# Optimization experiments

Measured on AMD Instinct MI355X. Metric: run time of the kernel, lower is better.

## Reference

```python
import jax, jax.numpy as jnp
import numpy as np

H = 1024
B = 8
T = 2048

def setup_inputs() -> dict:
    key = jax.random.key(0)
    ks = jax.random.split(key, 12)
    s = 1.0 / np.sqrt(H)
    return {
        "x": jax.random.normal(ks[0], (B, T, H), dtype=jnp.float32),
        "time_decay": jax.random.normal(ks[1], (H,), dtype=jnp.float32) * 0.1,
        "time_first": jax.random.normal(ks[2], (H,), dtype=jnp.float32) * 0.1,
        "time_mix_key": jax.random.uniform(ks[3], (1, 1, H), dtype=jnp.float32),
        "time_mix_value": jax.random.uniform(ks[4], (1, 1, H), dtype=jnp.float32),
        "time_mix_receptance": jax.random.uniform(ks[5], (1, 1, H), dtype=jnp.float32),
        "Wk": jax.random.normal(ks[6], (H, H), dtype=jnp.float32) * s,
        "Wv": jax.random.normal(ks[7], (H, H), dtype=jnp.float32) * s,
        "Wr": jax.random.normal(ks[8], (H, H), dtype=jnp.float32) * s,
        "Wo": jax.random.normal(ks[9], (H, H), dtype=jnp.float32) * s,
        "bo": jax.random.normal(ks[10], (H,), dtype=jnp.float32) * 0.01,
    }

def reference(x, time_decay, time_first, time_mix_key, time_mix_value,
              time_mix_receptance, Wk, Wv, Wr, Wo, bo):
    # time shift: shifted[:, t] = x[:, t-1], shifted[:, 0] = 0
    shifted = jnp.pad(x, ((0, 0), (1, 0), (0, 0)))[:, :-1]
    k_in = x * time_mix_key + shifted * (1.0 - time_mix_key)
    v_in = x * time_mix_value + shifted * (1.0 - time_mix_value)
    r_in = x * time_mix_receptance + shifted * (1.0 - time_mix_receptance)
    k = jnp.einsum('bth,oh->bto', k_in, Wk)
    v = jnp.einsum('bth,oh->bto', v_in, Wv)
    r = jax.nn.sigmoid(jnp.einsum('bth,oh->bto', r_in, Wr))

    td = jnp.exp(-jnp.exp(time_decay))  # (H,)

    def step(carry, kv):
        num, den = carry            # (B, H) each
        k_t, v_t = kv               # (B, H) each
        e = jnp.exp(time_first + k_t)
        out_t = (num + e * v_t) / (den + e)
        ek = jnp.exp(k_t)
        return (td * num + ek * v_t, td * den + ek), out_t

    init = (jnp.zeros((x.shape[0], x.shape[2]), x.dtype),
            jnp.zeros((x.shape[0], x.shape[2]), x.dtype))
    # scan over time: (T, B, H)
    _, wkv = jax.lax.scan(step, init, (k.transpose(1, 0, 2), v.transpose(1, 0, 2)))
    wkv = wkv.transpose(1, 0, 2)    # (B, T, H)

    return jnp.einsum('bth,oh->bto', r * wkv, Wo) + bo
```

## Files before the change

kernel.cpp:

```cpp
#include <hip/hip_runtime.h>
#include <hip/hip_bf16.h>
#include <cstdint>
#include <cstddef>

#define HH 1024
#define BB 8
#define TT 2048
#define MM (BB*TT)
#define CC 128
#define LL (TT/CC)

typedef __attribute__((ext_vector_type(8))) short bf16x8;
typedef __attribute__((ext_vector_type(8))) unsigned short u16x8;
typedef __attribute__((ext_vector_type(4))) float f32x4;

__device__ __forceinline__ unsigned short f2bf(float f) {
  union { float f; unsigned u; } v; v.f = f;
  return (unsigned short)((v.u + 0x7fffu + ((v.u >> 16) & 1u)) >> 16);
}
__device__ __forceinline__ float bf2f(unsigned short s) {
  union { float f; unsigned u; } v; v.u = ((unsigned)s) << 16;
  return v.f;
}

__device__ __forceinline__ void load_lds16(const void* g, void* l) {
  __builtin_amdgcn_global_load_lds((const __attribute__((address_space(1))) void*)g,
                                   (__attribute__((address_space(3))) void*)l,
                                   16, 0, 0);
}

__global__ __launch_bounds__(256) void prep(const float* __restrict__ x,
    const float* __restrict__ tmk, const float* __restrict__ tmv, const float* __restrict__ tmr,
    const float* __restrict__ Wk, const float* __restrict__ Wv,
    const float* __restrict__ Wr, const float* __restrict__ Wo,
    unsigned short* __restrict__ kin, unsigned short* __restrict__ vin,
    unsigned short* __restrict__ rin, unsigned short* __restrict__ Wbf) {
  const int bx = blockIdx.x;
  if (bx < 16384) {
    const int gid = bx * 256 + threadIdx.x;
    const size_t e0 = (size_t)gid * 4;
    const int h = (int)(e0 & (HH - 1));
    const int t = (int)((e0 >> 10) & (TT - 1));
    const float4 xv = *(const float4*)(x + e0);
    float4 sv = make_float4(0.f, 0.f, 0.f, 0.f);
    if (t != 0) sv = *(const float4*)(x + e0 - HH);
    const float4 k4 = *(const float4*)(tmk + h);
    const float4 v4 = *(const float4*)(tmv + h);
    const float4 r4 = *(const float4*)(tmr + h);
    ushort4 ko, vo, ro;
    ko.x = f2bf(sv.x + k4.x * (xv.x - sv.x)); ko.y = f2bf(sv.y + k4.y * (xv.y - sv.y));
    ko.z = f2bf(sv.z + k4.z * (xv.z - sv.z)); ko.w = f2bf(sv.w + k4.w * (xv.w - sv.w));
    vo.x = f2bf(sv.x + v4.x * (xv.x - sv.x)); vo.y = f2bf(sv.y + v4.y * (xv.y - sv.y));
    vo.z = f2bf(sv.z + v4.z * (xv.z - sv.z)); vo.w = f2bf(sv.w + v4.w * (xv.w - sv.w));
    ro.x = f2bf(sv.x + r4.x * (xv.x - sv.x)); ro.y = f2bf(sv.y + r4.y * (xv.y - sv.y));
    ro.z = f2bf(sv.z + r4.z * (xv.z - sv.z)); ro.w = f2bf(sv.w + r4.w * (xv.w - sv.w));
    *(ushort4*)(kin + e0) = ko;
    *(ushort4*)(vin + e0) = vo;
    *(ushort4*)(rin + e0) = ro;
  } else {
    const int q = bx - 16384;
    const int zz = q >> 10;
    const float* src = zz == 0 ? Wk : zz == 1 ? Wv : zz == 2 ? Wr : Wo;
    const int i = ((q & 1023) * 256 + threadIdx.x) * 4;
    const float4 v = *(const float4*)(src + i);
    ushort4 o; o.x = f2bf(v.x); o.y = f2bf(v.y); o.z = f2bf(v.z); o.w = f2bf(v.w);
    *(ushort4*)(Wbf + (size_t)zz * HH * HH + i) = o;
  }
}


#define BAR()   do { asm volatile("" ::: "memory"); __builtin_amdgcn_s_barrier(); \
                     asm volatile("" ::: "memory"); } while (0)
#define VM6()   asm volatile("s_waitcnt vmcnt(6)" ::: "memory")
#define VM0()   asm volatile("s_waitcnt vmcnt(0)" ::: "memory")
#define PRIO1() __builtin_amdgcn_s_setprio(1)
#define PRIO0() __builtin_amdgcn_s_setprio(0)

__device__ __forceinline__ void stA(const unsigned short* __restrict__ Ag, int m0, int kt,
                                    unsigned short* buf, int h, int w, int rl, int scol) {
#pragma unroll
  for (int l = 0; l < 2; ++l) {
    const int row = l * 128 + h * 64 + w * 8;
    load_lds16(Ag + (size_t)(m0 + row + rl) * HH + kt + scol, buf + row * 64);
  }
}
__device__ __forceinline__ void stB(const unsigned short* __restrict__ Bg, int n0, int kt,
                                    unsigned short* buf, int h, int w, int rl, int scol) {
#pragma unroll
  for (int l = 0; l < 2; ++l) {
    const int row = (2 * (l * 2 + (w >> 2)) + h) * 32 + (w & 3) * 8;
    load_lds16(Bg + (size_t)(n0 + row + rl) * HH + kt + scol, buf + row * 64);
  }
}

template<int MH>
__device__ __forceinline__ void rdA(const unsigned short* buf, bf16x8 (&af)[4][2],
                                    int wm, int l15, int kq, int swz) {
#pragma unroll
  for (int kk = 0; kk < 2; ++kk)
#pragma unroll
    for (int fm = 0; fm < 4; ++fm)
      af[fm][kk] = *(const bf16x8*)(buf + (wm * 128 + MH * 64 + fm * 16 + l15) * 64
                                        + ((kk * 32 + kq * 8) ^ swz));
}
template<int NH>
__device__ __forceinline__ void rdB(const unsigned short* buf, bf16x8 (&bfr)[2][2][2],
                                    int wn, int l15, int kq, int swz) {
#pragma unroll
  for (int kk = 0; kk < 2; ++kk)
#pragma unroll
    for (int fn = 0; fn < 2; ++fn)
      bfr[NH][fn][kk] = *(const bf16x8*)(buf + (wn * 64 + NH * 32 + fn * 16 + l15) * 64
                                             + ((kk * 32 + kq * 8) ^ swz));
}
template<int MH, int NH>
__device__ __forceinline__ void mfmaQ(f32x4 (&acc)[8][4], const bf16x8 (&af)[4][2],
                                      const bf16x8 (&bfr)[2][2][2]) {
#pragma unroll
  for (int kk = 0; kk < 2; ++kk)
#pragma unroll
    for (int fm = 0; fm < 4; ++fm)
#pragma unroll
      for (int fn = 0; fn < 2; ++fn)
        acc[MH * 4 + fm][NH * 2 + fn] = __builtin_amdgcn_mfma_f32_16x16x32_bf16(
            bfr[NH][fn][kk], af[fm][kk], acc[MH * 4 + fm][NH * 2 + fn], 0, 0, 0);
}

__device__ __forceinline__ void gemm256(const unsigned short* __restrict__ Ag,
                                        const unsigned short* __restrict__ Bg,
                                        const int m0, const int n0,
                                        unsigned short* As, unsigned short* Bs,
                                        f32x4 (&acc)[8][4]) {
  const int tid = threadIdx.x;
  const int lane = tid & 63;
  const int w = tid >> 6;
  const int wm = w >> 2, wn = w & 3;
  const int l15 = lane & 15, kq = lane >> 4;
  const int swz = (l15 & 7) << 3;
  const int rl = lane >> 3;
  const int scol = ((lane & 7) ^ rl) * 8;
  unsigned short* const A0 = As;
  unsigned short* const A1 = As + 256 * 64;
  unsigned short* const B0 = Bs;
  unsigned short* const B1 = Bs + 256 * 64;
  bf16x8 af[4][2], bfr[2][2][2];

  stA(Ag, m0, 0, A0, 0, w, rl, scol);
  stB(Bg, n0, 0, B0, 0, w, rl, scol);
  stB(Bg, n0, 0, B0, 1, w, rl, scol);
  stA(Ag, m0, 0, A0, 1, w, rl, scol);
  stA(Ag, m0, 64, A1, 0, w, rl, scol);
  stB(Bg, n0, 64, B1, 0, w, rl, scol);
  stB(Bg, n0, 64, B1, 1, w, rl, scol);
  VM6(); BAR();

#pragma unroll 1
  for (int i = 0; i < 8; ++i) {
    const int tb1 = ((2 * i + 1) * 64) & (HH - 1);
    const int tn0 = ((2 * i + 2) * 64) & (HH - 1);
    const int tn1 = ((2 * i + 3) * 64) & (HH - 1);
    rdB<0>(B0, bfr, wn, l15, kq, swz);
    rdA<0>(A0, af, wm, l15, kq, swz);
    stA(Ag, m0, tb1, A1, 1, w, rl, scol);
    BAR(); PRIO1(); mfmaQ<0, 0>(acc, af, bfr); PRIO0(); BAR();
    rdB<1>(B0, bfr, wn, l15, kq, swz);
    stA(Ag, m0, tn0, A0, 0, w, rl, scol);
    BAR(); PRIO1(); mfmaQ<0, 1>(acc, af, bfr); PRIO0(); BAR();
    rdA<1>(A0, af, wm, l15, kq, swz);
    stB(Bg, n0, tn0, B0, 0, w, rl, scol);
    BAR(); PRIO1(); mfmaQ<1, 1>(acc, af, bfr); PRIO0(); BAR();
    stB(Bg, n0, tn0, B0, 1, w, rl, scol);
    VM6(); BAR(); PRIO1(); mfmaQ<1, 0>(acc, af, bfr); PRIO0(); BAR();
    rdB<0>(B1, bfr, wn, l15, kq, swz);
    rdA<0>(A1, af, wm, l15, kq, swz);
    stA(Ag, m0, tn0, A0, 1, w, rl, scol);
    BAR(); PRIO1(); mfmaQ<0, 0>(acc, af, bfr); PRIO0(); BAR();
    rdB<1>(B1, bfr, wn, l15, kq, swz);
    stA(Ag, m0, tn1, A1, 0, w, rl, scol);
    BAR(); PRIO1(); mfmaQ<0, 1>(acc, af, bfr); PRIO0(); BAR();
    rdA<1>(A1, af, wm, l15, kq, swz);
    stB(Bg, n0, tn1, B1, 0, w, rl, scol);
    BAR(); PRIO1(); mfmaQ<1, 1>(acc, af, bfr); PRIO0(); BAR();
    stB(Bg, n0, tn1, B1, 1, w, rl, scol);
    VM6(); BAR(); PRIO1(); mfmaQ<1, 0>(acc, af, bfr); PRIO0(); BAR();
  }
  VM0();
}

__device__ __forceinline__ void swizzle_mn256(int x, int& m0, int& n0) {
  const int wg = (x & 7) * 32 + (x >> 3);
  m0 = (wg >> 2) * 256;
  n0 = (wg & 3) * 256;
}

__global__ __launch_bounds__(512, 2) void gemm_kvr(const unsigned short* __restrict__ kin,
    const unsigned short* __restrict__ vin, const unsigned short* __restrict__ rin,
    const unsigned short* __restrict__ Wbf,
    unsigned short* __restrict__ kb, unsigned short* __restrict__ vb,
    unsigned short* __restrict__ rb) {
  __shared__ unsigned short As[2 * 256 * 64];
  __shared__ unsigned short Bs[2 * 256 * 64];
  const int z = blockIdx.y;
  const unsigned short* Ag = z == 0 ? kin : (z == 1 ? vin : rin);
  const unsigned short* Bg = Wbf + (size_t)z * HH * HH;
  unsigned short* Cg = z == 0 ? kb : (z == 1 ? vb : rb);
  int m0, n0; swizzle_mn256(blockIdx.x, m0, n0);
  f32x4 acc[8][4] = {};
  gemm256(Ag, Bg, m0, n0, As, Bs, acc);
  const int lane = threadIdx.x & 63, w = threadIdx.x >> 6;
  const int wm = w >> 2, wn = w & 3, l15 = lane & 15, lq = lane >> 4;
  const bool sig = (z == 2);
#pragma unroll
  for (int fm = 0; fm < 8; ++fm) {
    const size_t mrow = (size_t)(m0 + wm * 128 + fm * 16 + l15) * HH;
#pragma unroll
    for (int fn = 0; fn < 4; ++fn) {
      const int ncol = n0 + wn * 64 + fn * 16 + lq * 4;
      float v0 = acc[fm][fn][0], v1 = acc[fm][fn][1];
      float v2 = acc[fm][fn][2], v3 = acc[fm][fn][3];
      if (sig) {
        v0 = 1.0f / (1.0f + __expf(-v0)); v1 = 1.0f / (1.0f + __expf(-v1));
        v2 = 1.0f / (1.0f + __expf(-v2)); v3 = 1.0f / (1.0f + __expf(-v3));
      }
      ushort4 o; o.x = f2bf(v0); o.y = f2bf(v1); o.z = f2bf(v2); o.w = f2bf(v3);
      *(ushort4*)(Cg + mrow + ncol) = o;
    }
  }
}

__global__ __launch_bounds__(512, 2) void gemm_o(const unsigned short* __restrict__ Ag,
    const unsigned short* __restrict__ Bg, const float* __restrict__ bias,
    float* __restrict__ C) {
  __shared__ unsigned short As[2 * 256 * 64];
  __shared__ unsigned short Bs[2 * 256 * 64];
  int m0, n0; swizzle_mn256(blockIdx.x, m0, n0);
  f32x4 acc[8][4] = {};
  gemm256(Ag, Bg, m0, n0, As, Bs, acc);
  const int lane = threadIdx.x & 63, w = threadIdx.x >> 6;
  const int wm = w >> 2, wn = w & 3, l15 = lane & 15, lq = lane >> 4;
#pragma unroll
  for (int fm = 0; fm < 8; ++fm) {
    const size_t mrow = (size_t)(m0 + wm * 128 + fm * 16 + l15) * HH;
#pragma unroll
    for (int fn = 0; fn < 4; ++fn) {
      const int ncol = n0 + wn * 64 + fn * 16 + lq * 4;
      const float4 bv = *(const float4*)(bias + ncol);
      float4 ov;
      ov.x = acc[fm][fn][0] + bv.x; ov.y = acc[fm][fn][1] + bv.y;
      ov.z = acc[fm][fn][2] + bv.z; ov.w = acc[fm][fn][3] + bv.w;
      *(float4*)(C + mrow + ncol) = ov;
    }
  }
}

__global__ __launch_bounds__(256) void wkv_part(const unsigned short* __restrict__ k,
    const unsigned short* __restrict__ v, const float* __restrict__ tdec,
    float* __restrict__ pnum, float* __restrict__ pden) {
  const int gid = blockIdx.x * 256 + threadIdx.x;
  const int h0 = (gid & 127) * 8;
  const int b = (gid >> 7) & (BB - 1);
  const int c = gid >> 10;
  float td[8], num[8], den[8];
#pragma unroll
  for (int j = 0; j < 8; ++j) {
    td[j] = __expf(-__expf(tdec[h0 + j]));
    num[j] = 0.f; den[j] = 0.f;
  }
  size_t idx = (size_t)b * TT * HH + (size_t)(c * LL) * HH + h0;
#pragma unroll 4
  for (int i = 0; i < LL; ++i, idx += HH) {
    const u16x8 k8 = *(const u16x8*)(k + idx);
    const u16x8 v8 = *(const u16x8*)(v + idx);
#pragma unroll
    for (int j = 0; j < 8; ++j) {
      const float ek = __expf(bf2f(k8[j]));
      num[j] = td[j] * num[j] + ek * bf2f(v8[j]);
      den[j] = td[j] * den[j] + ek;
    }
  }
  const size_t o = (size_t)c * (BB * HH) + b * HH + h0;
#pragma unroll
  for (int j = 0; j < 8; ++j) { pnum[o + j] = num[j]; pden[o + j] = den[j]; }
}

__global__ __launch_bounds__(256) void wkv_scan(const float* __restrict__ tdec,
    float* __restrict__ pnum, float* __restrict__ pden) {
  const int bh = blockIdx.x * 256 + threadIdx.x;
  const int h = bh & (HH - 1);
  const float ed = __expf(tdec[h]);
  const float tdL = __expf(-ed * (float)LL);
  float num = 0.f, den = 0.f;
#pragma unroll 8
  for (int c = 0; c < CC; ++c) {
    const size_t o = (size_t)c * (BB * HH) + bh;
    const float tn = pnum[o], td_ = pden[o];
    pnum[o] = num; pden[o] = den;
    num = tdL * num + tn;
    den = tdL * den + td_;
  }
}

__global__ __launch_bounds__(256) void wkv_final(const unsigned short* __restrict__ k,
    const unsigned short* __restrict__ v, const unsigned short* __restrict__ r,
    const float* __restrict__ tdec, const float* __restrict__ tfst,
    const float* __restrict__ pnum, const float* __restrict__ pden,
    unsigned short* __restrict__ rwkv) {
  const int gid = blockIdx.x * 256 + threadIdx.x;
  const int h0 = (gid & 127) * 8;
  const int b = (gid >> 7) & (BB - 1);
  const int c = gid >> 10;
  float td[8], etf[8], num[8], den[8];
  const size_t o = (size_t)c * (BB * HH) + b * HH + h0;
#pragma unroll
  for (int j = 0; j < 8; ++j) {
    td[j] = __expf(-__expf(tdec[h0 + j]));
    etf[j] = __expf(tfst[h0 + j]);
    num[j] = pnum[o + j]; den[j] = pden[o + j];
  }
  size_t idx = (size_t)b * TT * HH + (size_t)(c * LL) * HH + h0;
#pragma unroll 2
  for (int i = 0; i < LL; ++i, idx += HH) {
    const u16x8 k8 = *(const u16x8*)(k + idx);
    const u16x8 v8 = *(const u16x8*)(v + idx);
    const u16x8 r8 = *(const u16x8*)(r + idx);
    u16x8 o8;
#pragma unroll
    for (int j = 0; j < 8; ++j) {
      const float ek = __expf(bf2f(k8[j]));
      const float vt = bf2f(v8[j]);
      const float rt = bf2f(r8[j]);
      const float e = ek * etf[j];
      const float inv = __builtin_amdgcn_rcpf(den[j] + e);
      const float outv = (num[j] + e * vt) * inv;
      num[j] = td[j] * num[j] + ek * vt;
      den[j] = td[j] * den[j] + ek;
      o8[j] = f2bf(outv * rt);
    }
    *(u16x8*)(rwkv + idx) = o8;
  }
}

extern "C" void kernel_launch(void* const* d_in, const int* in_sizes, int n_in,
                              void* d_out, int out_size, void* d_ws, size_t ws_size,
                              hipStream_t stream) {
  (void)in_sizes; (void)n_in; (void)out_size; (void)ws_size;
  const float* x    = (const float*)d_in[0];
  const float* tdec = (const float*)d_in[1];
  const float* tfst = (const float*)d_in[2];
  const float* tmk  = (const float*)d_in[3];
  const float* tmv  = (const float*)d_in[4];
  const float* tmr  = (const float*)d_in[5];
  const float* Wk   = (const float*)d_in[6];
  const float* Wv   = (const float*)d_in[7];
  const float* Wr   = (const float*)d_in[8];
  const float* Wo   = (const float*)d_in[9];
  const float* bo   = (const float*)d_in[10];
  float* out = (float*)d_out;

  char* ws = (char*)d_ws;
  const size_t MiB = (size_t)1 << 20;
  unsigned short* Wbf = (unsigned short*)(ws);
  unsigned short* kin = (unsigned short*)(ws + 8 * MiB);
  unsigned short* vin = (unsigned short*)(ws + 40 * MiB);
  unsigned short* rin = (unsigned short*)(ws + 72 * MiB);
  unsigned short* rb  = (unsigned short*)(ws + 104 * MiB);
  unsigned short* kb = (unsigned short*)out;
  unsigned short* vb = kb + (size_t)MM * HH;
  unsigned short* rwkv = kin;
  float* pnum = (float*)(ws + 40 * MiB);
  float* pden = (float*)(ws + 44 * MiB);

  hipLaunchKernelGGL(prep, dim3(20480), dim3(256), 0, stream,
                     x, tmk, tmv, tmr, Wk, Wv, Wr, Wo, kin, vin, rin, Wbf);
  hipLaunchKernelGGL(gemm_kvr, dim3(256, 3), dim3(512), 0, stream,
                     kin, vin, rin, Wbf, kb, vb, rb);
  hipLaunchKernelGGL(wkv_part, dim3(512), dim3(256), 0, stream,
                     kb, vb, tdec, pnum, pden);
  hipLaunchKernelGGL(wkv_scan, dim3(32), dim3(256), 0, stream,
                     tdec, pnum, pden);
  hipLaunchKernelGGL(wkv_final, dim3(512), dim3(256), 0, stream,
                     kb, vb, rb, tdec, tfst, pnum, pden, rwkv);
  hipLaunchKernelGGL(gemm_o, dim3(256), dim3(512), 0, stream,
                     rwkv, Wbf + (size_t)3 * HH * HH, bo, out);
}
```

Baseline: 360.8 us.

## Split prep into weight-conversion and time-mix kernels; drop GEMM pre-MFMA barriers

The combined prep kernel becomes two kernels. conv_w converts the four weight matrices to bf16. mix_kernel walks 16 consecutive timesteps per thread and carries the previous x row in a register, so each x element is read once instead of twice for the time shift. Separately, the GEMM main loop removes the barrier before each MFMA quad and moves the vmcnt wait after the MFMAs, which reduces synchronisation stalls. That second change risks LDS read/write hazards if the remaining barriers no longer cover the double-buffer reuse.

```diff
diff --git a/kernel.cpp b/kernel.cpp
--- a/kernel.cpp
+++ b/kernel.cpp
@@ -29,24 +29,32 @@
                                    16, 0, 0);
 }
 
-__global__ __launch_bounds__(256) void prep(const float* __restrict__ x,
+__global__ __launch_bounds__(256) void conv_w(const float* __restrict__ Wk,
+    const float* __restrict__ Wv, const float* __restrict__ Wr,
+    const float* __restrict__ Wo, unsigned short* __restrict__ dst) {
+  const int i = (blockIdx.x * 256 + threadIdx.x) * 4;
+  const float* src = blockIdx.y == 0 ? Wk : blockIdx.y == 1 ? Wv : blockIdx.y == 2 ? Wr : Wo;
+  const float4 v = *(const float4*)(src + i);
+  ushort4 o; o.x = f2bf(v.x); o.y = f2bf(v.y); o.z = f2bf(v.z); o.w = f2bf(v.w);
+  *(ushort4*)(dst + (size_t)blockIdx.y * HH * HH + i) = o;
+}
+
+__global__ __launch_bounds__(256) void mix_kernel(const float* __restrict__ x,
     const float* __restrict__ tmk, const float* __restrict__ tmv, const float* __restrict__ tmr,
-    const float* __restrict__ Wk, const float* __restrict__ Wv,
-    const float* __restrict__ Wr, const float* __restrict__ Wo,
     unsigned short* __restrict__ kin, unsigned short* __restrict__ vin,
-    unsigned short* __restrict__ rin, unsigned short* __restrict__ Wbf) {
-  const int bx = blockIdx.x;
-  if (bx < 16384) {
-    const int gid = bx * 256 + threadIdx.x;
-    const size_t e0 = (size_t)gid * 4;
-    const int h = (int)(e0 & (HH - 1));
-    const int t = (int)((e0 >> 10) & (TT - 1));
-    const float4 xv = *(const float4*)(x + e0);
-    float4 sv = make_float4(0.f, 0.f, 0.f, 0.f);
-    if (t != 0) sv = *(const float4*)(x + e0 - HH);
-    const float4 k4 = *(const float4*)(tmk + h);
-    const float4 v4 = *(const float4*)(tmv + h);
-    const float4 r4 = *(const float4*)(tmr + h);
+    unsigned short* __restrict__ rin) {
+  const int b = blockIdx.x >> 7;
+  const int t0 = (blockIdx.x & 127) * 16;
+  const int h = threadIdx.x * 4;
+  const float4 k4 = *(const float4*)(tmk + h);
+  const float4 v4 = *(const float4*)(tmv + h);
+  const float4 r4 = *(const float4*)(tmr + h);
+  size_t base = (size_t)b * TT * HH + (size_t)t0 * HH + h;
+  float4 sv = make_float4(0.f, 0.f, 0.f, 0.f);
+  if (t0 != 0) sv = *(const float4*)(x + base - HH);
+#pragma unroll 4
+  for (int i = 0; i < 16; ++i) {
+    const float4 xv = *(const float4*)(x + base);
     ushort4 ko, vo, ro;
     ko.x = f2bf(sv.x + k4.x * (xv.x - sv.x)); ko.y = f2bf(sv.y + k4.y * (xv.y - sv.y));
     ko.z = f2bf(sv.z + k4.z * (xv.z - sv.z)); ko.w = f2bf(sv.w + k4.w * (xv.w - sv.w));
@@ -54,17 +62,10 @@
     vo.z = f2bf(sv.z + v4.z * (xv.z - sv.z)); vo.w = f2bf(sv.w + v4.w * (xv.w - sv.w));
     ro.x = f2bf(sv.x + r4.x * (xv.x - sv.x)); ro.y = f2bf(sv.y + r4.y * (xv.y - sv.y));
     ro.z = f2bf(sv.z + r4.z * (xv.z - sv.z)); ro.w = f2bf(sv.w + r4.w * (xv.w - sv.w));
-    *(ushort4*)(kin + e0) = ko;
-    *(ushort4*)(vin + e0) = vo;
-    *(ushort4*)(rin + e0) = ro;
-  } else {
-    const int q = bx - 16384;
-    const int zz = q >> 10;
-    const float* src = zz == 0 ? Wk : zz == 1 ? Wv : zz == 2 ? Wr : Wo;
-    const int i = ((q & 1023) * 256 + threadIdx.x) * 4;
-    const float4 v = *(const float4*)(src + i);
-    ushort4 o; o.x = f2bf(v.x); o.y = f2bf(v.y); o.z = f2bf(v.z); o.w = f2bf(v.w);
-    *(ushort4*)(Wbf + (size_t)zz * HH * HH + i) = o;
+    *(ushort4*)(kin + base) = ko;
+    *(ushort4*)(vin + base) = vo;
+    *(ushort4*)(rin + base) = ro;
+    sv = xv; base += HH;
   }
 }
 
@@ -162,27 +163,27 @@
     rdB<0>(B0, bfr, wn, l15, kq, swz);
     rdA<0>(A0, af, wm, l15, kq, swz);
     stA(Ag, m0, tb1, A1, 1, w, rl, scol);
-    BAR(); PRIO1(); mfmaQ<0, 0>(acc, af, bfr); PRIO0(); BAR();
+    PRIO1(); mfmaQ<0, 0>(acc, af, bfr); PRIO0(); BAR();
     rdB<1>(B0, bfr, wn, l15, kq, swz);
     stA(Ag, m0, tn0, A0, 0, w, rl, scol);
-    BAR(); PRIO1(); mfmaQ<0, 1>(acc, af, bfr); PRIO0(); BAR();
+    PRIO1(); mfmaQ<0, 1>(acc, af, bfr); PRIO0(); BAR();
     rdA<1>(A0, af, wm, l15, kq, swz);
     stB(Bg, n0, tn0, B0, 0, w, rl, scol);
-    BAR(); PRIO1(); mfmaQ<1, 1>(acc, af, bfr); PRIO0(); BAR();
+    PRIO1(); mfmaQ<1, 1>(acc, af, bfr); PRIO0(); BAR();
     stB(Bg, n0, tn0, B0, 1, w, rl, scol);
-    VM6(); BAR(); PRIO1(); mfmaQ<1, 0>(acc, af, bfr); PRIO0(); BAR();
+    PRIO1(); mfmaQ<1, 0>(acc, af, bfr); PRIO0(); VM6(); BAR();
     rdB<0>(B1, bfr, wn, l15, kq, swz);
     rdA<0>(A1, af, wm, l15, kq, swz);
     stA(Ag, m0, tn0, A0, 1, w, rl, scol);
-    BAR(); PRIO1(); mfmaQ<0, 0>(acc, af, bfr); PRIO0(); BAR();
+    PRIO1(); mfmaQ<0, 0>(acc, af, bfr); PRIO0(); BAR();
     rdB<1>(B1, bfr, wn, l15, kq, swz);
     stA(Ag, m0, tn1, A1, 0, w, rl, scol);
-    BAR(); PRIO1(); mfmaQ<0, 1>(acc, af, bfr); PRIO0(); BAR();
+    PRIO1(); mfmaQ<0, 1>(acc, af, bfr); PRIO0(); BAR();
     rdA<1>(A1, af, wm, l15, kq, swz);
     stB(Bg, n0, tn1, B1, 0, w, rl, scol);
-    BAR(); PRIO1(); mfmaQ<1, 1>(acc, af, bfr); PRIO0(); BAR();
+    PRIO1(); mfmaQ<1, 1>(acc, af, bfr); PRIO0(); BAR();
     stB(Bg, n0, tn1, B1, 1, w, rl, scol);
-    VM6(); BAR(); PRIO1(); mfmaQ<1, 0>(acc, af, bfr); PRIO0(); BAR();
+    PRIO1(); mfmaQ<1, 0>(acc, af, bfr); PRIO0(); VM6(); BAR();
   }
   VM0();
 }
@@ -370,8 +371,9 @@
   float* pnum = (float*)(ws + 40 * MiB);
   float* pden = (float*)(ws + 44 * MiB);
 
-  hipLaunchKernelGGL(prep, dim3(20480), dim3(256), 0, stream,
-                     x, tmk, tmv, tmr, Wk, Wv, Wr, Wo, kin, vin, rin, Wbf);
+  hipLaunchKernelGGL(conv_w, dim3(1024, 4), dim3(256), 0, stream, Wk, Wv, Wr, Wo, Wbf);
+  hipLaunchKernelGGL(mix_kernel, dim3(1024), dim3(256), 0, stream,
+                     x, tmk, tmv, tmr, kin, vin, rin);
   hipLaunchKernelGGL(gemm_kvr, dim3(256, 3), dim3(512), 0, stream,
                      kin, vin, rin, Wbf, kb, vb, rb);
   hipLaunchKernelGGL(wkv_part, dim3(512), dim3(256), 0, stream,
```

Result: faster. 348.6 us (-3.4%).
